# Kernel optimization log

Measured on AMD Instinct MI355X. Metric: run time of the kernel, lower is better.

Reference implementation:

```python
import jax, jax.numpy as jnp
import numpy as np
import math

DIM = 256
B, T = 4, 4096

def setup_inputs() -> dict:
    key = jax.random.key(0)
    ks = jax.random.split(key, 16)
    d = DIM
    def lin(k, dout, din):
        bound = 1.0 / math.sqrt(din)
        kw, kb = jax.random.split(k)
        W = jax.random.uniform(kw, (dout, din), minval=-bound, maxval=bound, dtype=jnp.float32)
        b = jax.random.uniform(kb, (dout,), minval=-bound, maxval=bound, dtype=jnp.float32)
        return W, b
    x = jax.random.normal(ks[0], (B, T, d), dtype=jnp.float32)
    wq, bq = lin(ks[1], d, d)
    wk, bk = lin(ks[2], d, d)
    wv, bv = lin(ks[3], d, d)
    wo, bo = lin(ks[4], d, d)
    w1, b1 = lin(ks[5], 4 * d, d)
    w2, b2 = lin(ks[6], d, 4 * d)
    return {
        "x": x,
        "attn_norm_w": jnp.ones((d,), jnp.float32),
        "mlp_norm_w": jnp.ones((d,), jnp.float32),
        "wq": wq, "bq": bq, "wk": wk, "bk": bk, "wv": wv, "bv": bv,
        "wo": wo, "bo": bo, "w1": w1, "b1": b1, "w2": w2, "b2": b2,
    }

def _rms_norm(x, w, eps=1e-6):
    rms = jnp.sqrt(jnp.mean(x * x, axis=-1, keepdims=True) + eps)
    return x / rms * w

def reference(x, attn_norm_w, mlp_norm_w, wq, bq, wk, bk, wv, bv, wo, bo, w1, b1, w2, b2):
    b, t, d = x.shape
    xn = _rms_norm(x, attn_norm_w)
    q = xn @ wq.T + bq  # [b,t,d]
    k = xn @ wk.T + bk
    v = xn @ wv.T + bv
    scores = jnp.einsum('btd,bsd->bts', q, k) / math.sqrt(d)
    causal = jnp.tril(jnp.ones((t, t), dtype=bool))
    scores = jnp.where(causal, scores, -1e9)
    probs = jax.nn.softmax(scores, axis=-1)
    attn = jnp.einsum('bts,bsd->btd', probs, v)
    x = x + attn @ wo.T + bo
    hn = _rms_norm(x, mlp_norm_w)
    h = jax.nn.gelu(hn @ w1.T + b1, approximate=False)
    return x + h @ w2.T + b2
```

## Files before the change

kernel.cpp:

```cpp
#include <hip/hip_runtime.h>

typedef __attribute__((ext_vector_type(8))) short bfrag;
typedef __attribute__((ext_vector_type(4))) float f32x4;

__device__ __forceinline__ f32x4 mfma16(bfrag a, bfrag b, f32x4 c) {
    return __builtin_amdgcn_mfma_f32_16x16x32_bf16(a, b, c, 0, 0, 0);
}
__device__ __forceinline__ unsigned short f2bf(float f) {
    unsigned int u = __float_as_uint(f);
    u = u + 0x7fffu + ((u >> 16) & 1u);
    return (unsigned short)(u >> 16);
}
__device__ __forceinline__ void glds16(const unsigned short* g, unsigned short* l) {
    __builtin_amdgcn_global_load_lds(
        (const __attribute__((address_space(1))) void*)g,
        (__attribute__((address_space(3))) void*)l, 16, 0, 0);
}

#define DIM 256
#define BT  16384
#define TSEQ 4096
#define FB   1048576


__global__ __launch_bounds__(256) void k_prep(
    const float* __restrict__ x, const float* __restrict__ anw,
    const float* __restrict__ wq, const float* __restrict__ wk,
    const float* __restrict__ wv, const float* __restrict__ wo,
    const float* __restrict__ w1, const float* __restrict__ w2,
    unsigned short* __restrict__ wqF, unsigned short* __restrict__ wkF,
    unsigned short* __restrict__ wvF, unsigned short* __restrict__ woF,
    unsigned short* __restrict__ w1F, unsigned short* __restrict__ w2F,
    unsigned short* __restrict__ xnF)
{
    int bid = blockIdx.x;
    int wave = threadIdx.x >> 6, lane = threadIdx.x & 63;
    int q = lane >> 4, r = lane & 15;
    if (bid < 384) {
        int fid = bid * 4 + wave;
        const float* src; unsigned short* dst; int ntile, ks, K, fbase;
        if (fid < 512) {
            int w = fid >> 7, fl = fid & 127;
            ntile = fl >> 3; ks = fl & 7; K = 256;
            src = (w == 0) ? wq : (w == 1) ? wk : (w == 2) ? wv : wo;
            dst = (w == 0) ? wqF : (w == 1) ? wkF : (w == 2) ? wvF : woF;
            fbase = (ntile * 8 + ks) * 512;
        } else if (fid < 1024) {
            int fl = fid - 512;
            ntile = fl >> 3; ks = fl & 7; K = 256;
            src = w1; dst = w1F;
            fbase = (ntile * 8 + ks) * 512;
        } else {
            int fl = fid - 1024;
            ntile = fl >> 5; ks = fl & 31; K = 1024;
            src = w2; dst = w2F;
            fbase = (ntile * 32 + ks) * 512;
        }
        const float* s = src + (ntile * 16 + r) * K + ks * 32 + q * 8;
        float4 v0 = *(const float4*)(s);
        float4 v1 = *(const float4*)(s + 4);
        unsigned short o[8] = { f2bf(v0.x), f2bf(v0.y), f2bf(v0.z), f2bf(v0.w),
                                f2bf(v1.x), f2bf(v1.y), f2bf(v1.z), f2bf(v1.w) };
        *(ushort4*)(dst + fbase + lane * 8)     = make_ushort4(o[0], o[1], o[2], o[3]);
        *(ushort4*)(dst + fbase + lane * 8 + 4) = make_ushort4(o[4], o[5], o[6], o[7]);
    } else {
        int row  = (bid - 384) * 4 + wave;
        float4 v = *(const float4*)(x + row * DIM + lane * 4);
        float ss = v.x*v.x + v.y*v.y + v.z*v.z + v.w*v.w;
        #pragma unroll
        for (int off = 1; off < 64; off <<= 1) ss += __shfl_xor(ss, off);
        float inv = rsqrtf(ss * (1.0f / DIM) + 1e-6f);
        float4 w = *(const float4*)(anw + lane * 4);
        ushort4 o = make_ushort4(f2bf(v.x*inv*w.x), f2bf(v.y*inv*w.y),
                                 f2bf(v.z*inv*w.z), f2bf(v.w*inv*w.w));
        int c = lane * 4;
        int ks = c >> 5, qp = (c >> 3) & 3, e0 = c & 7;
        *(ushort4*)(xnF + (((row >> 4) * 8 + ks) * 512) + ((qp * 16 + (row & 15)) * 8) + e0) = o;
    }
}


__global__ __launch_bounds__(256) void k_qkv(
    const unsigned short* __restrict__ xnF,
    const unsigned short* __restrict__ wqF, const unsigned short* __restrict__ wkF,
    const unsigned short* __restrict__ wvF,
    const float* __restrict__ bq, const float* __restrict__ bk, const float* __restrict__ bv,
    unsigned short* __restrict__ Q, unsigned short* __restrict__ KF,
    unsigned short* __restrict__ VF)
{
    __shared__ __align__(16) unsigned short sb[2][20 * 512];
    int bid = blockIdx.x;
    int wave = threadIdx.x >> 6, lane = threadIdx.x & 63;
    int m0 = (bid / 3) * 64;
    int grp = bid % 3;
    int nc  = wave * 64;
    const unsigned short* WF = (grp == 0) ? wqF : (grp == 1) ? wkF : wvF;
    const float* bias        = (grp == 0) ? bq  : (grp == 1) ? bk  : bv;
    int q = lane >> 4, r = lane & 15;
    int lane8 = lane * 8;
    int mt = m0 >> 4;

    #define QKV_STAGE(ks, buf)                                                   \
        { int _k = (ks);                                                         \
          _Pragma("unroll")                                                      \
          for (int t = 0; t < 5; ++t) {                                          \
              int f = wave * 5 + t;                                              \
              const unsigned short* g = (f < 4)                                  \
                  ? xnF + ((mt + f) * 8 + _k) * 512                              \
                  : WF  + ((f - 4) * 8 + _k) * 512;                              \
              glds16(g + lane8, &sb[buf][f * 512]);                              \
          } }

    f32x4 acc[4][4] = {};
    QKV_STAGE(0, 0)
    for (int ks = 0; ks < 8; ++ks) {
        int cur = ks & 1;
        if (ks + 1 < 8) { QKV_STAGE(ks + 1, cur ^ 1) }
        if (ks + 1 < 8) asm volatile("s_waitcnt vmcnt(5)" ::: "memory");
        else            asm volatile("s_waitcnt vmcnt(0)" ::: "memory");
        asm volatile("s_barrier" ::: "memory");
        bfrag a[4], b[4];
        #pragma unroll
        for (int i = 0; i < 4; ++i) a[i] = *(const bfrag*)(&sb[cur][i * 512] + lane8);
        #pragma unroll
        for (int j = 0; j < 4; ++j) b[j] = *(const bfrag*)(&sb[cur][(4 + wave * 4 + j) * 512] + lane8);
        #pragma unroll
        for (int i = 0; i < 4; ++i)
            #pragma unroll
            for (int j = 0; j < 4; ++j) acc[i][j] = mfma16(a[i], b[j], acc[i][j]);
        asm volatile("s_barrier" ::: "memory");
    }
    #undef QKV_STAGE

    if (grp == 0) {
        #pragma unroll
        for (int j = 0; j < 4; ++j) {
            int col = nc + j * 16 + r;
            float bz = bias[col];
            #pragma unroll
            for (int i = 0; i < 4; ++i)
                #pragma unroll
                for (int g = 0; g < 4; ++g) {
                    int row = m0 + i * 16 + q * 4 + g;
                    Q[row * DIM + col] = f2bf(acc[i][j][g] + bz);
                }
        }
    } else if (grp == 1) {
        #pragma unroll
        for (int j = 0; j < 4; ++j) {
            int col = nc + j * 16 + r;
            int ks = col >> 5, qc = (col >> 3) & 3, e = col & 7;
            float bz = bias[col];
            #pragma unroll
            for (int i = 0; i < 4; ++i)
                #pragma unroll
                for (int g = 0; g < 4; ++g) {
                    int row = m0 + i * 16 + q * 4 + g;
                    int bb = row >> 12;
                    int r5 = row & 31, tile = (row & 4095) >> 5;
                    int h = (r5 >> 2) & 1;
                    int rc = ((r5 >> 3) << 2) | (r5 & 3);
                    KF[bb * FB + (tile * 16 + ks * 2 + h) * 512 + (qc * 16 + rc) * 8 + e]
                        = f2bf(acc[i][j][g] + bz);
                }
        }
    } else {
        #pragma unroll
        for (int j = 0; j < 4; ++j) {
            int vd = nc + j * 16 + r;
            int jc = vd >> 4, rc = vd & 15;
            float bz = bias[vd];
            #pragma unroll
            for (int i = 0; i < 4; ++i) {
                int t0 = m0 + i * 16 + q * 4;
                int bb = t0 >> 12, tl = t0 & (TSEQ - 1);
                int tile = tl >> 5, qc = (tl >> 3) & 3, e0 = tl & 7;
                ushort4 o = make_ushort4(f2bf(acc[i][j][0] + bz), f2bf(acc[i][j][1] + bz),
                                         f2bf(acc[i][j][2] + bz), f2bf(acc[i][j][3] + bz));
                *(ushort4*)(VF + bb * FB + (tile * 16 + jc) * 512 + (qc * 16 + rc) * 8 + e0) = o;
            }
        }
    }
}

__global__ __launch_bounds__(128, 1) void k_attn(
    const unsigned short* __restrict__ Q, const unsigned short* __restrict__ KF,
    const unsigned short* __restrict__ VF, unsigned short* __restrict__ AOF)
{
    __shared__ __align__(16) unsigned char arena[65536];
    int bid = blockIdx.x;
    int xcd = bid & 7;
    int batch = xcd >> 1;
    int qt = 255 - (((bid >> 3) << 1) | (xcd & 1));
    int wave = threadIdx.x >> 6;
    int lane = threadIdx.x & 63;
    int q = lane >> 4, r = lane & 15;
    int q0 = qt * 16;
    const unsigned short* Qb  = Q  + (size_t)batch * TSEQ * DIM;
    const unsigned short* KFb = KF + (size_t)batch * FB;
    const unsigned short* VFb = VF + (size_t)batch * FB;
    int lane8 = lane * 8;

    unsigned short* Kl = (unsigned short*)(arena + wave * 32768);
    unsigned short* Vl = Kl + 8192;

    bfrag qf[8];
    #pragma unroll
    for (int ks = 0; ks < 8; ++ks)
        qf[ks] = *(const bfrag*)(Qb + (q0 + r) * DIM + ks * 32 + q * 8);

    f32x4 o[16] = {};
    float lsum = 0.f;

    int ktiles = (q0 + 16 + 31) >> 5;
    int half = ktiles >> 1, rem = ktiles & 1;
    int cnt   = half + (wave == 0 ? rem : 0);
    int start = (wave == 0) ? 0 : half + rem;

    if (cnt > 0) {
        const unsigned short* kg = KFb + (size_t)start * 8192;
        #pragma unroll
        for (int f = 0; f < 16; ++f) glds16(kg + f * 512 + lane8, Kl + f * 512);
        const unsigned short* vg = VFb + (size_t)start * 8192;
        #pragma unroll
        for (int j = 0; j < 16; ++j) glds16(vg + j * 512 + lane8, Vl + j * 512);
    }

    for (int i = 0; i < cnt; ++i) {
        int kt = start + i;
        bool more = (i + 1 < cnt);
        asm volatile("s_waitcnt vmcnt(16)" ::: "memory");
        bfrag kb0[8], kb1[8];
        #pragma unroll
        for (int ks = 0; ks < 8; ++ks) {
            kb0[ks] = *(const bfrag*)(Kl + (ks * 2    ) * 512 + lane8);
            kb1[ks] = *(const bfrag*)(Kl + (ks * 2 + 1) * 512 + lane8);
        }
        f32x4 s0 = {}, s1 = {};
        #pragma unroll
        for (int ks = 0; ks < 8; ++ks) {
            s0 = mfma16(kb0[ks], qf[ks], s0);
            s1 = mfma16(kb1[ks], qf[ks], s1);
        }
        if (more) {
            asm volatile("s_waitcnt lgkmcnt(0)" ::: "memory");
            const unsigned short* kg = KFb + (size_t)(kt + 1) * 8192;
            #pragma unroll
            for (int f = 0; f < 16; ++f) glds16(kg + f * 512 + lane8, Kl + f * 512);
        }
        int kk0 = kt * 32;
        bool lastt = (kt == ktiles - 1);
        int qglob = q0 + r;
        bfrag pf;
        #pragma unroll
        for (int g = 0; g < 4; ++g) {
            int key0 = kk0 + q * 8 + g;
            float p0 = (lastt && key0     > qglob) ? 0.f : __expf(s0[g] * 0.0625f);
            float p1 = (lastt && key0 + 4 > qglob) ? 0.f : __expf(s1[g] * 0.0625f);
            lsum += p0 + p1;
            pf[g]     = (short)f2bf(p0);
            pf[g + 4] = (short)f2bf(p1);
        }
        if (more) asm volatile("s_waitcnt vmcnt(16)" ::: "memory");
        else      asm volatile("s_waitcnt vmcnt(0)"  ::: "memory");
        #pragma unroll
        for (int j = 0; j < 16; ++j) {
            bfrag vb = *(const bfrag*)(Vl + j * 512 + lane8);
            o[j] = mfma16(pf, vb, o[j]);
        }
        if (more) {
            asm volatile("s_waitcnt lgkmcnt(0)" ::: "memory");
            const unsigned short* vg = VFb + (size_t)(kt + 1) * 8192;
            #pragma unroll
            for (int j = 0; j < 16; ++j) glds16(vg + j * 512 + lane8, Vl + j * 512);
        }
    }

    lsum += __shfl_xor(lsum, 16);
    lsum += __shfl_xor(lsum, 32);
    __syncthreads();
    float* Obuf = (float*)arena;
    float* Lbuf = (float*)(arena + 16 * 260 * 4);
    if (wave == 0) {
        if (lane < 16) Lbuf[lane] = lsum;
        #pragma unroll
        for (int j = 0; j < 16; ++j)
            #pragma unroll
            for (int g = 0; g < 4; ++g)
                Obuf[(q * 4 + g) * 260 + j * 16 + r] = o[j][g];
    }
    __syncthreads();
    if (wave == 1) {
        if (lane < 16) Lbuf[lane] += lsum;
        #pragma unroll
        for (int j = 0; j < 16; ++j)
            #pragma unroll
            for (int g = 0; g < 4; ++g)
                Obuf[(q * 4 + g) * 260 + j * 16 + r] += o[j][g];
    }
    __syncthreads();

    float linv[4];
    #pragma unroll
    for (int g = 0; g < 4; ++g) linv[g] = 1.0f / Lbuf[q * 4 + g];
    unsigned short* AOt = AOF + (size_t)(batch * 256 + qt) * 8 * 512;
    #pragma unroll
    for (int jj = 0; jj < 8; ++jj) {
        int j = wave * 8 + jj;
        int d = j * 16 + r;
        int ks = d >> 5, qp = (d >> 3) & 3, e = d & 7;
        #pragma unroll
        for (int g = 0; g < 4; ++g)
            AOt[ks * 512 + (qp * 16 + q * 4 + g) * 8 + e] =
                f2bf(Obuf[(q * 4 + g) * 260 + j * 16 + r] * linv[g]);
    }
}

__global__ __launch_bounds__(256) void k_wo(
    const unsigned short* __restrict__ AOF, const unsigned short* __restrict__ woF,
    const float* __restrict__ bo, const float* __restrict__ x,
    const float* __restrict__ mnw, float* __restrict__ x2,
    unsigned short* __restrict__ hnF)
{
    __shared__ __align__(16) unsigned short sb[2][20 * 512];
    int bid = blockIdx.x;
    int wave = threadIdx.x >> 6, lane = threadIdx.x & 63;
    int m0 = bid * 64 + wave * 16;
    int mt = bid * 4 + wave;
    int mtB = bid * 4;
    int q = lane >> 4, r = lane & 15;
    int lane8 = lane * 8;

    #define WO_STAGE(ks, buf)                                                    \
        { int _k = (ks);                                                         \
          _Pragma("unroll")                                                      \
          for (int t = 0; t < 5; ++t) {                                          \
              int f = wave * 5 + t;                                              \
              const unsigned short* g = (f < 4)                                  \
                  ? AOF + ((mtB + f) * 8 + _k) * 512                             \
                  : woF + ((f - 4) * 8 + _k) * 512;                              \
              glds16(g + lane8, &sb[buf][f * 512]);                              \
          } }

    f32x4 acc[16] = {};
    WO_STAGE(0, 0)
    for (int ks = 0; ks < 8; ++ks) {
        int cur = ks & 1;
        if (ks + 1 < 8) { WO_STAGE(ks + 1, cur ^ 1) }
        if (ks + 1 < 8) asm volatile("s_waitcnt vmcnt(5)" ::: "memory");
        else            asm volatile("s_waitcnt vmcnt(0)" ::: "memory");
        asm volatile("s_barrier" ::: "memory");
        bfrag a = *(const bfrag*)(&sb[cur][wave * 512] + lane8);
        #pragma unroll
        for (int j = 0; j < 16; ++j) {
            bfrag b = *(const bfrag*)(&sb[cur][(4 + j) * 512] + lane8);
            acc[j] = mfma16(a, b, acc[j]);
        }
        asm volatile("s_barrier" ::: "memory");
    }
    #undef WO_STAGE

    float ss[4] = {0.f, 0.f, 0.f, 0.f};
    #pragma unroll
    for (int j = 0; j < 16; ++j) {
        int n = j * 16 + r;
        float bz = bo[n];
        #pragma unroll
        for (int g = 0; g < 4; ++g) {
            int row = m0 + q * 4 + g;
            float v = acc[j][g] + bz + x[row * DIM + n];
            acc[j][g] = v;
            ss[g] += v * v;
            x2[row * DIM + n] = v;
        }
    }
    #pragma unroll
    for (int g = 0; g < 4; ++g) {
        #pragma unroll
        for (int off = 1; off < 16; off <<= 1) ss[g] += __shfl_xor(ss[g], off);
    }
    #pragma unroll
    for (int j = 0; j < 16; ++j) {
        int n = j * 16 + r;
        int ks = n >> 5, qp = (n >> 3) & 3, e = n & 7;
        float wn = mnw[n];
        #pragma unroll
        for (int g = 0; g < 4; ++g) {
            float inv = rsqrtf(ss[g] * (1.0f / DIM) + 1e-6f);
            hnF[(mt * 8 + ks) * 512 + (qp * 16 + q * 4 + g) * 8 + e]
                = f2bf(acc[j][g] * inv * wn);
        }
    }
}

__global__ __launch_bounds__(256) void k_w1(
    const unsigned short* __restrict__ hnF, const unsigned short* __restrict__ w1F,
    const float* __restrict__ b1, unsigned short* __restrict__ hF)
{
    __shared__ __align__(16) unsigned short sb[2][20 * 512];
    int bid = blockIdx.x;
    int wave = threadIdx.x >> 6, lane = threadIdx.x & 63;
    int m0 = (bid >> 2) * 64;
    int n0 = (bid & 3) * 256 + wave * 64;
    int mt = m0 >> 4, ntb = (bid & 3) * 16;
    int q = lane >> 4, r = lane & 15;
    int lane8 = lane * 8;

    #define W1_STAGE(ks, buf)                                                    \
        { int _k = (ks);                                                         \
          _Pragma("unroll")                                                      \
          for (int t = 0; t < 5; ++t) {                                          \
              int f = wave * 5 + t;                                              \
              const unsigned short* g = (f < 4)                                  \
                  ? hnF + ((mt + f) * 8 + _k) * 512                              \
                  : w1F + ((ntb + f - 4) * 8 + _k) * 512;                        \
              glds16(g + lane8, &sb[buf][f * 512]);                              \
          } }

    f32x4 acc[4][4] = {};
    W1_STAGE(0, 0)
    for (int ks = 0; ks < 8; ++ks) {
        int cur = ks & 1;
        if (ks + 1 < 8) { W1_STAGE(ks + 1, cur ^ 1) }
        if (ks + 1 < 8) asm volatile("s_waitcnt vmcnt(5)" ::: "memory");
        else            asm volatile("s_waitcnt vmcnt(0)" ::: "memory");
        asm volatile("s_barrier" ::: "memory");
        bfrag a[4], b[4];
        #pragma unroll
        for (int i = 0; i < 4; ++i) a[i] = *(const bfrag*)(&sb[cur][i * 512] + lane8);
        #pragma unroll
        for (int j = 0; j < 4; ++j) b[j] = *(const bfrag*)(&sb[cur][(4 + wave * 4 + j) * 512] + lane8);
        #pragma unroll
        for (int i = 0; i < 4; ++i)
            #pragma unroll
            for (int j = 0; j < 4; ++j) acc[i][j] = mfma16(a[i], b[j], acc[i][j]);
        asm volatile("s_barrier" ::: "memory");
    }
    #undef W1_STAGE

    #pragma unroll
    for (int j = 0; j < 4; ++j) {
        int n = n0 + j * 16 + r;
        int ks = n >> 5, qp = (n >> 3) & 3, e = n & 7;
        float bz = b1[n];
        #pragma unroll
        for (int i = 0; i < 4; ++i)
            #pragma unroll
            for (int g = 0; g < 4; ++g) {
                float v = acc[i][j][g] + bz;
                float ge = 0.5f * v * (1.0f + erff(v * 0.70710678118654752f));
                hF[((mt + i) * 32 + ks) * 512 + (qp * 16 + q * 4 + g) * 8 + e] = f2bf(ge);
            }
    }
}

__global__ __launch_bounds__(256) void k_w2(
    const unsigned short* __restrict__ hF, const unsigned short* __restrict__ w2F,
    const float* __restrict__ b2, const float* __restrict__ x2,
    float* __restrict__ out)
{
    __shared__ __align__(16) unsigned short sb[2][20 * 512];
    int bid = blockIdx.x;
    int wave = threadIdx.x >> 6, lane = threadIdx.x & 63;
    int m0 = bid * 64;
    int n0 = wave * 64;
    int mt = m0 >> 4;
    int q = lane >> 4, r = lane & 15;
    int lane8 = lane * 8;

    #define W2_STAGE(ks, buf)                                                    \
        { int _k = (ks);                                                         \
          _Pragma("unroll")                                                      \
          for (int t = 0; t < 5; ++t) {                                          \
              int f = wave * 5 + t;                                              \
              const unsigned short* g = (f < 4)                                  \
                  ? hF  + ((mt + f) * 32 + _k) * 512                             \
                  : w2F + ((f - 4) * 32 + _k) * 512;                             \
              glds16(g + lane8, &sb[buf][f * 512]);                              \
          } }

    f32x4 acc[4][4] = {};
    W2_STAGE(0, 0)
    for (int ks = 0; ks < 32; ++ks) {
        int cur = ks & 1;
        if (ks + 1 < 32) { W2_STAGE(ks + 1, cur ^ 1) }
        if (ks + 1 < 32) asm volatile("s_waitcnt vmcnt(5)" ::: "memory");
        else             asm volatile("s_waitcnt vmcnt(0)" ::: "memory");
        asm volatile("s_barrier" ::: "memory");
        bfrag a[4], b[4];
        #pragma unroll
        for (int i = 0; i < 4; ++i) a[i] = *(const bfrag*)(&sb[cur][i * 512] + lane8);
        #pragma unroll
        for (int j = 0; j < 4; ++j) b[j] = *(const bfrag*)(&sb[cur][(4 + wave * 4 + j) * 512] + lane8);
        #pragma unroll
        for (int i = 0; i < 4; ++i)
            #pragma unroll
            for (int j = 0; j < 4; ++j) acc[i][j] = mfma16(a[i], b[j], acc[i][j]);
        asm volatile("s_barrier" ::: "memory");
    }
    #undef W2_STAGE

    #pragma unroll
    for (int j = 0; j < 4; ++j) {
        int n = n0 + j * 16 + r;
        float bz = b2[n];
        #pragma unroll
        for (int i = 0; i < 4; ++i)
            #pragma unroll
            for (int g = 0; g < 4; ++g) {
                int row = m0 + i * 16 + q * 4 + g;
                out[row * DIM + n] = acc[i][j][g] + bz + x2[row * DIM + n];
            }
    }
}

#define OFF_WQB 0u
#define OFF_WKB 131072u
#define OFF_WVB 262144u
#define OFF_WOB 393216u
#define OFF_W1B 524288u
#define OFF_W2B 1048576u
#define OFF_XN  1572864u
#define OFF_Q   9961472u
#define OFF_KF  18350080u
#define OFF_VF  26738688u
#define OFF_AO  35127296u
#define OFF_X2  43515904u
#define OFF_HN  60293120u
#define OFF_H   OFF_XN

extern "C" void kernel_launch(void* const* d_in, const int* in_sizes, int n_in,
                              void* d_out, int out_size, void* d_ws, size_t ws_size,
                              hipStream_t stream) {
    const float* x   = (const float*)d_in[0];
    const float* anw = (const float*)d_in[1];
    const float* mnw = (const float*)d_in[2];
    const float* wq  = (const float*)d_in[3];
    const float* bq  = (const float*)d_in[4];
    const float* wk  = (const float*)d_in[5];
    const float* bk  = (const float*)d_in[6];
    const float* wv  = (const float*)d_in[7];
    const float* bv  = (const float*)d_in[8];
    const float* wo  = (const float*)d_in[9];
    const float* bo  = (const float*)d_in[10];
    const float* w1  = (const float*)d_in[11];
    const float* b1  = (const float*)d_in[12];
    const float* w2  = (const float*)d_in[13];
    const float* b2  = (const float*)d_in[14];
    float* out = (float*)d_out;

    char* ws = (char*)d_ws;
    unsigned short* wqF = (unsigned short*)(ws + OFF_WQB);
    unsigned short* wkF = (unsigned short*)(ws + OFF_WKB);
    unsigned short* wvF = (unsigned short*)(ws + OFF_WVB);
    unsigned short* woF = (unsigned short*)(ws + OFF_WOB);
    unsigned short* w1F = (unsigned short*)(ws + OFF_W1B);
    unsigned short* w2F = (unsigned short*)(ws + OFF_W2B);
    unsigned short* xnF = (unsigned short*)(ws + OFF_XN);
    unsigned short* Qp  = (unsigned short*)(ws + OFF_Q);
    unsigned short* KFp = (unsigned short*)(ws + OFF_KF);
    unsigned short* VFp = (unsigned short*)(ws + OFF_VF);
    unsigned short* AOF = (unsigned short*)(ws + OFF_AO);
    float*          x2  = (float*)         (ws + OFF_X2);
    unsigned short* hnF = (unsigned short*)(ws + OFF_HN);
    unsigned short* hFp = (unsigned short*)(ws + OFF_H);

    k_prep<<<dim3(4480), dim3(256), 0, stream>>>(x, anw, wq, wk, wv, wo, w1, w2,
                                                 wqF, wkF, wvF, woF, w1F, w2F, xnF);
    k_qkv <<<dim3(768),  dim3(256), 0, stream>>>(xnF, wqF, wkF, wvF, bq, bk, bv, Qp, KFp, VFp);
    k_attn<<<dim3(1024), dim3(128), 0, stream>>>(Qp, KFp, VFp, AOF);
    k_wo  <<<dim3(256),  dim3(256), 0, stream>>>(AOF, woF, bo, x, mnw, x2, hnF);
    k_w1  <<<dim3(1024), dim3(256), 0, stream>>>(hnF, w1F, b1, hFp);
    k_w2  <<<dim3(256),  dim3(256), 0, stream>>>(hFp, w2F, b2, x2, out);
}
```

Before: 281.4 us.

## Process 32 query rows per single-wave attention block, dropping the cross-wave key split

The attention kernel now uses one wave per block that handles two 16-row query tiles against every key tile. This reuses each loaded K/V tile for twice as many queries and removes the two-wave key split along with its LDS reduction and barriers. Q is written by the QKV kernel in the fragment layout so it can be loaded directly as MFMA operands. In exchange there are half as many blocks and a much longer serial key loop per block, which lowers parallelism and raises register pressure from the doubled accumulators.

Measured after the change: 388.5 us. +38.1%, slower.

```diff
diff --git a/kernel.cpp b/kernel.cpp
--- a/kernel.cpp
+++ b/kernel.cpp
@@ -79,13 +79,12 @@
     }
 }
 
-
 __global__ __launch_bounds__(256) void k_qkv(
     const unsigned short* __restrict__ xnF,
     const unsigned short* __restrict__ wqF, const unsigned short* __restrict__ wkF,
     const unsigned short* __restrict__ wvF,
     const float* __restrict__ bq, const float* __restrict__ bk, const float* __restrict__ bv,
-    unsigned short* __restrict__ Q, unsigned short* __restrict__ KF,
+    unsigned short* __restrict__ QF, unsigned short* __restrict__ KF,
     unsigned short* __restrict__ VF)
 {
     __shared__ __align__(16) unsigned short sb[2][20 * 512];
@@ -136,13 +135,15 @@
         #pragma unroll
         for (int j = 0; j < 4; ++j) {
             int col = nc + j * 16 + r;
+            int ks = col >> 5, qp = (col >> 3) & 3, e = col & 7;
             float bz = bias[col];
             #pragma unroll
             for (int i = 0; i < 4; ++i)
                 #pragma unroll
                 for (int g = 0; g < 4; ++g) {
                     int row = m0 + i * 16 + q * 4 + g;
-                    Q[row * DIM + col] = f2bf(acc[i][j][g] + bz);
+                    QF[((row >> 4) * 8 + ks) * 512 + (qp * 16 + (row & 15)) * 8 + e]
+                        = f2bf(acc[i][j][g] + bz);
                 }
         }
     } else if (grp == 1) {
@@ -183,64 +184,52 @@
     }
 }
 
-__global__ __launch_bounds__(128, 1) void k_attn(
-    const unsigned short* __restrict__ Q, const unsigned short* __restrict__ KF,
+__global__ __launch_bounds__(64, 1) void k_attn(
+    const unsigned short* __restrict__ QF, const unsigned short* __restrict__ KF,
     const unsigned short* __restrict__ VF, unsigned short* __restrict__ AOF)
 {
-    __shared__ __align__(16) unsigned char arena[65536];
+    __shared__ __align__(16) unsigned short Kl[8192];
+    __shared__ __align__(16) unsigned short Vl[8192];
+    __shared__ float Lb[2][16];
     int bid = blockIdx.x;
     int xcd = bid & 7;
     int batch = xcd >> 1;
-    int qt = 255 - (((bid >> 3) << 1) | (xcd & 1));
-    int wave = threadIdx.x >> 6;
-    int lane = threadIdx.x & 63;
+    int qt = 127 - (((bid >> 3) << 1) | (xcd & 1));
+    int lane = threadIdx.x;
     int q = lane >> 4, r = lane & 15;
-    int q0 = qt * 16;
-    const unsigned short* Qb  = Q  + (size_t)batch * TSEQ * DIM;
+    int q0 = qt * 32;
     const unsigned short* KFb = KF + (size_t)batch * FB;
     const unsigned short* VFb = VF + (size_t)batch * FB;
     int lane8 = lane * 8;
 
-    unsigned short* Kl = (unsigned short*)(arena + wave * 32768);
-    unsigned short* Vl = Kl + 8192;
-
-    bfrag qf[8];
-    #pragma unroll
-    for (int ks = 0; ks < 8; ++ks)
-        qf[ks] = *(const bfrag*)(Qb + (q0 + r) * DIM + ks * 32 + q * 8);
-
-    f32x4 o[16] = {};
-    float lsum = 0.f;
-
-    int ktiles = (q0 + 16 + 31) >> 5;
-    int half = ktiles >> 1, rem = ktiles & 1;
-    int cnt   = half + (wave == 0 ? rem : 0);
-    int start = (wave == 0) ? 0 : half + rem;
-
-    if (cnt > 0) {
-        const unsigned short* kg = KFb + (size_t)start * 8192;
-        #pragma unroll
-        for (int f = 0; f < 16; ++f) glds16(kg + f * 512 + lane8, Kl + f * 512);
-        const unsigned short* vg = VFb + (size_t)start * 8192;
-        #pragma unroll
-        for (int j = 0; j < 16; ++j) glds16(vg + j * 512 + lane8, Vl + j * 512);
-    }
-
-    for (int i = 0; i < cnt; ++i) {
-        int kt = start + i;
-        bool more = (i + 1 < cnt);
+    bfrag qf[2][8];
+    #pragma unroll
+    for (int m = 0; m < 2; ++m)
+        #pragma unroll
+        for (int ks = 0; ks < 8; ++ks)
+            qf[m][ks] = *(const bfrag*)(QF + ((size_t)(batch * 256 + qt * 2 + m) * 8 + ks) * 512 + lane8);
+
+    f32x4 o[2][16] = {};
+    float lsum0 = 0.f, lsum1 = 0.f;
+    int ktiles = qt + 1;
+
+    #pragma unroll
+    for (int f = 0; f < 16; ++f) glds16(KFb + f * 512 + lane8, Kl + f * 512);
+    #pragma unroll
+    for (int j = 0; j < 16; ++j) glds16(VFb + j * 512 + lane8, Vl + j * 512);
+
+    for (int kt = 0; kt < ktiles; ++kt) {
+        bool more = (kt + 1 < ktiles);
         asm volatile("s_waitcnt vmcnt(16)" ::: "memory");
-        bfrag kb0[8], kb1[8];
+        f32x4 s00 = {}, s01 = {}, s10 = {}, s11 = {};
         #pragma unroll
         for (int ks = 0; ks < 8; ++ks) {
-            kb0[ks] = *(const bfrag*)(Kl + (ks * 2    ) * 512 + lane8);
-            kb1[ks] = *(const bfrag*)(Kl + (ks * 2 + 1) * 512 + lane8);
-        }
-        f32x4 s0 = {}, s1 = {};
-        #pragma unroll
-        for (int ks = 0; ks < 8; ++ks) {
-            s0 = mfma16(kb0[ks], qf[ks], s0);
-            s1 = mfma16(kb1[ks], qf[ks], s1);
+            bfrag kb0 = *(const bfrag*)(Kl + (ks * 2    ) * 512 + lane8);
+            bfrag kb1 = *(const bfrag*)(Kl + (ks * 2 + 1) * 512 + lane8);
+            s00 = mfma16(kb0, qf[0][ks], s00);
+            s10 = mfma16(kb0, qf[1][ks], s10);
+            s01 = mfma16(kb1, qf[0][ks], s01);
+            s11 = mfma16(kb1, qf[1][ks], s11);
         }
         if (more) {
             asm volatile("s_waitcnt lgkmcnt(0)" ::: "memory");
@@ -250,23 +239,27 @@
         }
         int kk0 = kt * 32;
         bool lastt = (kt == ktiles - 1);
-        int qglob = q0 + r;
-        bfrag pf;
+        bfrag pf0, pf1;
+        int qg0 = q0 + r, qg1 = q0 + 16 + r;
         #pragma unroll
         for (int g = 0; g < 4; ++g) {
             int key0 = kk0 + q * 8 + g;
-            float p0 = (lastt && key0     > qglob) ? 0.f : __expf(s0[g] * 0.0625f);
-            float p1 = (lastt && key0 + 4 > qglob) ? 0.f : __expf(s1[g] * 0.0625f);
-            lsum += p0 + p1;
-            pf[g]     = (short)f2bf(p0);
-            pf[g + 4] = (short)f2bf(p1);
+            float p00 = (lastt && key0     > qg0) ? 0.f : __expf(s00[g] * 0.0625f);
+            float p01 = (lastt && key0 + 4 > qg0) ? 0.f : __expf(s01[g] * 0.0625f);
+            float p10 = (lastt && key0     > qg1) ? 0.f : __expf(s10[g] * 0.0625f);
+            float p11 = (lastt && key0 + 4 > qg1) ? 0.f : __expf(s11[g] * 0.0625f);
+            lsum0 += p00 + p01;
+            lsum1 += p10 + p11;
+            pf0[g] = (short)f2bf(p00); pf0[g + 4] = (short)f2bf(p01);
+            pf1[g] = (short)f2bf(p10); pf1[g + 4] = (short)f2bf(p11);
         }
         if (more) asm volatile("s_waitcnt vmcnt(16)" ::: "memory");
         else      asm volatile("s_waitcnt vmcnt(0)"  ::: "memory");
         #pragma unroll
         for (int j = 0; j < 16; ++j) {
             bfrag vb = *(const bfrag*)(Vl + j * 512 + lane8);
-            o[j] = mfma16(pf, vb, o[j]);
+            o[0][j] = mfma16(pf0, vb, o[0][j]);
+            o[1][j] = mfma16(pf1, vb, o[1][j]);
         }
         if (more) {
             asm volatile("s_waitcnt lgkmcnt(0)" ::: "memory");
@@ -276,43 +269,24 @@
         }
     }
 
-    lsum += __shfl_xor(lsum, 16);
-    lsum += __shfl_xor(lsum, 32);
-    __syncthreads();
-    float* Obuf = (float*)arena;
-    float* Lbuf = (float*)(arena + 16 * 260 * 4);
-    if (wave == 0) {
-        if (lane < 16) Lbuf[lane] = lsum;
-        #pragma unroll
-        for (int j = 0; j < 16; ++j)
+    lsum0 += __shfl_xor(lsum0, 16); lsum0 += __shfl_xor(lsum0, 32);
+    lsum1 += __shfl_xor(lsum1, 16); lsum1 += __shfl_xor(lsum1, 32);
+    if (lane < 16) { Lb[0][lane] = lsum0; Lb[1][lane] = lsum1; }
+
+    #pragma unroll
+    for (int m = 0; m < 2; ++m) {
+        float linv[4];
+        #pragma unroll
+        for (int g = 0; g < 4; ++g) linv[g] = 1.0f / Lb[m][q * 4 + g];
+        unsigned short* AOt = AOF + (size_t)(batch * 256 + qt * 2 + m) * 8 * 512;
+        #pragma unroll
+        for (int j = 0; j < 16; ++j) {
+            int d = j * 16 + r;
+            int ks = d >> 5, qp = (d >> 3) & 3, e = d & 7;
             #pragma unroll
             for (int g = 0; g < 4; ++g)
-                Obuf[(q * 4 + g) * 260 + j * 16 + r] = o[j][g];
-    }
-    __syncthreads();
-    if (wave == 1) {
-        if (lane < 16) Lbuf[lane] += lsum;
-        #pragma unroll
-        for (int j = 0; j < 16; ++j)
-            #pragma unroll
-            for (int g = 0; g < 4; ++g)
-                Obuf[(q * 4 + g) * 260 + j * 16 + r] += o[j][g];
-    }
-    __syncthreads();
-
-    float linv[4];
-    #pragma unroll
-    for (int g = 0; g < 4; ++g) linv[g] = 1.0f / Lbuf[q * 4 + g];
-    unsigned short* AOt = AOF + (size_t)(batch * 256 + qt) * 8 * 512;
-    #pragma unroll
-    for (int jj = 0; jj < 8; ++jj) {
-        int j = wave * 8 + jj;
-        int d = j * 16 + r;
-        int ks = d >> 5, qp = (d >> 3) & 3, e = d & 7;
-        #pragma unroll
-        for (int g = 0; g < 4; ++g)
-            AOt[ks * 512 + (qp * 16 + q * 4 + g) * 8 + e] =
-                f2bf(Obuf[(q * 4 + g) * 260 + j * 16 + r] * linv[g]);
+                AOt[ks * 512 + (qp * 16 + q * 4 + g) * 8 + e] = f2bf(o[m][j][g] * linv[g]);
+        }
     }
 }
 
@@ -557,7 +531,7 @@
     unsigned short* w1F = (unsigned short*)(ws + OFF_W1B);
     unsigned short* w2F = (unsigned short*)(ws + OFF_W2B);
     unsigned short* xnF = (unsigned short*)(ws + OFF_XN);
-    unsigned short* Qp  = (unsigned short*)(ws + OFF_Q);
+    unsigned short* QFp = (unsigned short*)(ws + OFF_Q);
     unsigned short* KFp = (unsigned short*)(ws + OFF_KF);
     unsigned short* VFp = (unsigned short*)(ws + OFF_VF);
     unsigned short* AOF = (unsigned short*)(ws + OFF_AO);
@@ -567,8 +541,8 @@
 
     k_prep<<<dim3(4480), dim3(256), 0, stream>>>(x, anw, wq, wk, wv, wo, w1, w2,
                                                  wqF, wkF, wvF, woF, w1F, w2F, xnF);
-    k_qkv <<<dim3(768),  dim3(256), 0, stream>>>(xnF, wqF, wkF, wvF, bq, bk, bv, Qp, KFp, VFp);
-    k_attn<<<dim3(1024), dim3(128), 0, stream>>>(Qp, KFp, VFp, AOF);
+    k_qkv <<<dim3(768),  dim3(256), 0, stream>>>(xnF, wqF, wkF, wvF, bq, bk, bv, QFp, KFp, VFp);
+    k_attn<<<dim3(512),  dim3(64),  0, stream>>>(QFp, KFp, VFp, AOF);
     k_wo  <<<dim3(256),  dim3(256), 0, stream>>>(AOF, woF, bo, x, mnw, x2, hnF);
     k_w1  <<<dim3(1024), dim3(256), 0, stream>>>(hnF, w1F, b1, hFp);
     k_w2  <<<dim3(256),  dim3(256), 0, stream>>>(hFp, w2F, b2, x2, out);
```
